# Kernel tuning notes

Hardware: AMD Instinct MI355X
Metric: run time of the kernel (lower is better)

## Reference

```python
import jax, jax.numpy as jnp
import numpy as np


def setup_inputs() -> dict:
    key = jax.random.key(0)
    ks = jax.random.split(key, 8)
    bs, slen, d = 16, 2048, 1024
    scale = 1.0 / np.sqrt(d)
    return {
        "query": jax.random.normal(ks[0], (bs, d), jnp.float32),
        "states": jax.random.normal(ks[1], (bs, slen, d), jnp.float32),
        "Wq": jax.random.normal(ks[2], (d, d), jnp.float32) * scale,
        "bq": jax.random.normal(ks[3], (d,), jnp.float32) * 0.01,
        "Wk": jax.random.normal(ks[4], (d, d), jnp.float32) * scale,
        "bk": jax.random.normal(ks[5], (d,), jnp.float32) * 0.01,
        "We": jax.random.normal(ks[6], (2 * d,), jnp.float32) * scale,
        "be": jax.random.normal(ks[7], (1,), jnp.float32) * 0.01,
    }


def reference(query, states, Wq, bq, Wk, bk, We, be):
    d = Wq.shape[1]
    # q: (bs, d); k: (bs, slen, d)
    q = jax.nn.relu(query @ Wq + bq)
    k = jax.nn.relu(jnp.einsum("bsv,vd->bsd", states, Wk) + bk)
    # tanh(cat(q, k)) @ We == tanh(q) @ We[:d] + tanh(k) @ We[d:]
    # (avoids materializing the repeated/concatenated (bs, slen, 2d) tensor)
    We_q, We_k = We[:d], We[d:]
    energy = (jnp.tanh(q) @ We_q)[:, None] + jnp.einsum("bsd,d->bs", jnp.tanh(k), We_k) + be[0]
    attn_weights = jax.nn.softmax(energy, axis=1)  # (bs, slen)
    attn = jnp.einsum("bs,bsd->bd", attn_weights, states)  # weighted sum of values
    return attn_weights, attn
```

## Files before the change

kernel.cpp:

```cpp
#include <hip/hip_runtime.h>
#include <hip/hip_bf16.h>

#define D 1024
#define SLEN 2048
#define BS 16
#define MROWS (BS*SLEN)

typedef __attribute__((ext_vector_type(8))) short short8;
typedef __attribute__((ext_vector_type(4))) float f32x4;

__device__ __forceinline__ short f2bf(float f) {
  __hip_bfloat16 h = __float2bfloat16(f);
  return __builtin_bit_cast(short, h);
}

__device__ __forceinline__ float4 ntload4(const float* p) {
  f32x4 v = __builtin_nontemporal_load((const f32x4*)p);
  float4 r; r.x = v.x; r.y = v.y; r.z = v.z; r.w = v.w; return r;
}

__global__ __launch_bounds__(256) void wk_prep(const float* __restrict__ Wk,
                                               short* __restrict__ WkT) {
  const int g = blockIdx.x;
  const int t = threadIdx.x;
#pragma unroll
  for (int it = 0; it < 4; ++it) {
    const int n = it*256 + t;
    short8 p;
#pragma unroll
    for (int j = 0; j < 8; ++j)
      p[j] = f2bf(Wk[(size_t)(g*8 + j)*D + n]);
    *(short8*)(WkT + ((size_t)g*D + n)*8) = p;
  }
}

__global__ __launch_bounds__(512, 2) void energy_gemm(
    const float* __restrict__ states, const short* __restrict__ WkT,
    const float* __restrict__ bk, const float* __restrict__ We,
    float* __restrict__ eraw, float* __restrict__ attn)
{
  __shared__ short Al[64 * 129 * 8];

  const int tid  = threadIdx.x;
  const int w    = tid >> 6;
  const int lane = tid & 63;
  const int quad = lane >> 4;
  const int l16  = lane & 15;
  const int m0   = blockIdx.x * 64;

  if (blockIdx.x < BS && tid < 256) {
    f32x4 z = {0.f, 0.f, 0.f, 0.f};
    *(f32x4*)(attn + (size_t)blockIdx.x*D + tid*4) = z;
  }

  {
    const int row = tid >> 3;
    const int u0  = tid & 7;
    const float* Ag = states + (size_t)(m0 + row)*D;
#pragma unroll
    for (int i = 0; i < 16; ++i) {
      const int u = u0 + i*8;
      float4 x0 = ntload4(Ag + u*8);
      float4 x1 = ntload4(Ag + u*8 + 4);
      short8 p;
      p[0]=f2bf(x0.x); p[1]=f2bf(x0.y); p[2]=f2bf(x0.z); p[3]=f2bf(x0.w);
      p[4]=f2bf(x1.x); p[5]=f2bf(x1.y); p[6]=f2bf(x1.z); p[7]=f2bf(x1.w);
      *(short8*)(Al + ((size_t)row*129 + u)*8) = p;
    }
  }
  __syncthreads();

  f32x4 acc[2][4][4];
#pragma unroll
  for (int nc = 0; nc < 2; ++nc)
#pragma unroll
    for (int mi = 0; mi < 4; ++mi)
#pragma unroll
      for (int ni = 0; ni < 4; ++ni)
        acc[nc][mi][ni] = (f32x4){0.f, 0.f, 0.f, 0.f};

  const short* bbase = WkT + ((size_t)quad*D + w*128 + l16)*8;
  const short* abase = Al + ((size_t)l16*129 + quad)*8;

#define LOADB(ks, buf)                                                   \
  {                                                                      \
    const short* bp = bbase + (size_t)(ks)*32768;                        \
    _Pragma("unroll")                                                    \
    for (int nc = 0; nc < 2; ++nc)                                       \
      _Pragma("unroll")                                                  \
      for (int ni = 0; ni < 4; ++ni)                                     \
        buf[nc*4 + ni] = *(const short8*)(bp + nc*512 + ni*128);         \
  }

#define LOADA(ks, buf)                                                   \
  {                                                                      \
    _Pragma("unroll")                                                    \
    for (int mi = 0; mi < 4; ++mi)                                       \
      buf[mi] = *(const short8*)(abase + mi*16512 + (ks)*32);            \
  }

#define MFMAS(fa, fb)                                                    \
  {                                                                      \
    _Pragma("unroll")                                                    \
    for (int nc = 0; nc < 2; ++nc)                                       \
      _Pragma("unroll")                                                  \
      for (int mi = 0; mi < 4; ++mi)                                     \
        _Pragma("unroll")                                                \
        for (int ni = 0; ni < 4; ++ni)                                   \
          acc[nc][mi][ni] = __builtin_amdgcn_mfma_f32_16x16x32_bf16(     \
              fa[mi], fb[nc*4 + ni], acc[nc][mi][ni], 0, 0, 0);          \
  }

  short8 fa0[4], fa1[4], fb0[8], fb1[8];
  LOADA(0, fa0); LOADB(0, fb0);
#pragma unroll
  for (int kk = 0; kk < 16; ++kk) {
    LOADA(2*kk + 1, fa1); LOADB(2*kk + 1, fb1);
    MFMAS(fa0, fb0);
    if (kk < 15) { LOADA(2*kk + 2, fa0); LOADB(2*kk + 2, fb0); }
    MFMAS(fa1, fb1);
  }

  float esum[16];
#pragma unroll
  for (int q = 0; q < 16; ++q) esum[q] = 0.f;
#pragma unroll
  for (int nc = 0; nc < 2; ++nc)
#pragma unroll
    for (int ni = 0; ni < 4; ++ni) {
      const int n = w*128 + nc*64 + ni*16 + l16;
      const float bkv = bk[n];
      const float wev = We[D + n];
#pragma unroll
      for (int mi = 0; mi < 4; ++mi)
#pragma unroll
        for (int r = 0; r < 4; ++r) {
          float x = acc[nc][mi][ni][r] + bkv;
          x = fmaxf(x, 0.f);
          float ex = __expf(2.f * x);
          float th = 1.f - 2.f/(ex + 1.f);
          esum[mi*4 + r] += th * wev;
        }
    }
#pragma unroll
  for (int dd = 1; dd < 16; dd <<= 1)
#pragma unroll
    for (int q = 0; q < 16; ++q)
      esum[q] += __shfl_xor(esum[q], dd, 64);

  __syncthreads();
  float* red = (float*)Al;
  if (l16 == 0) {
#pragma unroll
    for (int mi = 0; mi < 4; ++mi)
#pragma unroll
      for (int r = 0; r < 4; ++r)
        red[(mi*16 + quad*4 + r)*8 + w] = esum[mi*4 + r];
  }
  __syncthreads();
  if (tid < 64) {
    float s = 0.f;
#pragma unroll
    for (int wi = 0; wi < 8; ++wi) s += red[tid*8 + wi];
    eraw[m0 + tid] = s;
  }
#undef LOADB
#undef LOADA
#undef MFMAS
}

__global__ __launch_bounds__(256) void attn_sm_partial(
    const float* __restrict__ states, const float* __restrict__ eraw,
    float* __restrict__ wts, float* __restrict__ attn)
{
  const int sc = blockIdx.x;
  const int b  = blockIdx.y;
  const int t  = threadIdx.x;
  __shared__ float red[256];
  __shared__ float wsh[128];

  float v[8];
  float m = -1e30f;
#pragma unroll
  for (int j = 0; j < 8; ++j) {
    v[j] = eraw[(size_t)b*SLEN + j*256 + t];
    m = fmaxf(m, v[j]);
  }
  red[t] = m; __syncthreads();
  for (int s = 128; s > 0; s >>= 1) {
    if (t < s) red[t] = fmaxf(red[t], red[t+s]);
    __syncthreads();
  }
  m = red[0];
  __syncthreads();
  float sum = 0.f;
#pragma unroll
  for (int j = 0; j < 8; ++j) sum += __expf(v[j] - m);
  red[t] = sum; __syncthreads();
  for (int s = 128; s > 0; s >>= 1) {
    if (t < s) red[t] += red[t+s];
    __syncthreads();
  }
  const float inv = 1.f / red[0];

  if (t < 128) {
    const float wv = __expf(eraw[(size_t)b*SLEN + sc*128 + t] - m) * inv;
    wts[(size_t)b*SLEN + sc*128 + t] = wv;
    wsh[t] = wv;
  }
  __syncthreads();

  const float* sp = states + ((size_t)b*SLEN + sc*128)*D + t*4;
  float ax = 0.f, ay = 0.f, az = 0.f, aw = 0.f;
#pragma unroll 8
  for (int s = 0; s < 128; ++s) {
    float4 x = ntload4(sp + (size_t)s*D);
    const float wv = wsh[s];
    ax = fmaf(wv, x.x, ax);
    ay = fmaf(wv, x.y, ay);
    az = fmaf(wv, x.z, az);
    aw = fmaf(wv, x.w, aw);
  }
  float* o = attn + (size_t)b*D + t*4;
  atomicAdd(o+0, ax); atomicAdd(o+1, ay);
  atomicAdd(o+2, az); atomicAdd(o+3, aw);
}

extern "C" void kernel_launch(void* const* d_in, const int* in_sizes, int n_in,
                              void* d_out, int out_size, void* d_ws, size_t ws_size,
                              hipStream_t stream) {
  const float* states = (const float*)d_in[1];
  const float* Wk     = (const float*)d_in[4];
  const float* bk     = (const float*)d_in[5];
  const float* We     = (const float*)d_in[6];
  float* out = (float*)d_out;

  short* WkT  = (short*)d_ws;
  float* eraw = (float*)((char*)d_ws + (size_t)D*D*sizeof(short));

  (void)in_sizes; (void)n_in; (void)out_size; (void)ws_size;

  wk_prep<<<128, 256, 0, stream>>>(Wk, WkT);
  energy_gemm<<<MROWS/64, 512, 0, stream>>>(states, WkT, bk, We, eraw, out + MROWS);
  attn_sm_partial<<<dim3(16, BS), 256, 0, stream>>>(states, eraw, out, out + MROWS);
}
```

Baseline: 289.8 us.

## Split softmax from weighted sum and widen attention accumulation parallelism

Moves the per-batch softmax into its own small kernel so the weighted-sum kernel no longer recomputes the full softmax reduction in every block. The accumulation kernel now runs twice as many blocks, each with 512 threads covering two 32-row halves of a 64-row chunk, and combines the halves in shared memory before the atomics. States loads switch from nontemporal to normal loads, which may let them hit in cache after the GEMM pass. The cost is an extra kernel launch and a round trip of the weights through global memory.

New measurement: 301.7 us. 4.1% more time.

```diff
diff --git a/kernel.cpp b/kernel.cpp
--- a/kernel.cpp
+++ b/kernel.cpp
@@ -169,61 +169,81 @@
 #undef MFMAS
 }
 
-__global__ __launch_bounds__(256) void attn_sm_partial(
-    const float* __restrict__ states, const float* __restrict__ eraw,
-    float* __restrict__ wts, float* __restrict__ attn)
+__global__ __launch_bounds__(256) void softmax_w(
+    const float* __restrict__ eraw, float* __restrict__ wts)
+{
+  const int b = blockIdx.x;
+  const int t = threadIdx.x;
+  __shared__ float red[256];
+
+  float v[8];
+  float m = -1e30f;
+#pragma unroll
+  for (int j = 0; j < 8; ++j) {
+    v[j] = eraw[(size_t)b*SLEN + j*256 + t];
+    m = fmaxf(m, v[j]);
+  }
+  red[t] = m; __syncthreads();
+  for (int s = 128; s > 0; s >>= 1) {
+    if (t < s) red[t] = fmaxf(red[t], red[t+s]);
+    __syncthreads();
+  }
+  m = red[0];
+  __syncthreads();
+
+  float e[8];
+  float sum = 0.f;
+#pragma unroll
+  for (int j = 0; j < 8; ++j) { e[j] = __expf(v[j] - m); sum += e[j]; }
+  red[t] = sum; __syncthreads();
+  for (int s = 128; s > 0; s >>= 1) {
+    if (t < s) red[t] += red[t+s];
+    __syncthreads();
+  }
+  const float inv = 1.f / red[0];
+#pragma unroll
+  for (int j = 0; j < 8; ++j)
+    wts[(size_t)b*SLEN + j*256 + t] = e[j] * inv;
+}
+
+__global__ __launch_bounds__(512, 4) void attn_accum(
+    const float* __restrict__ states, const float* __restrict__ wts,
+    float* __restrict__ attn)
 {
   const int sc = blockIdx.x;
   const int b  = blockIdx.y;
   const int t  = threadIdx.x;
-  __shared__ float red[256];
-  __shared__ float wsh[128];
-
-  float v[8];
-  float m = -1e30f;
-#pragma unroll
-  for (int j = 0; j < 8; ++j) {
-    v[j] = eraw[(size_t)b*SLEN + j*256 + t];
-    m = fmaxf(m, v[j]);
-  }
-  red[t] = m; __syncthreads();
-  for (int s = 128; s > 0; s >>= 1) {
-    if (t < s) red[t] = fmaxf(red[t], red[t+s]);
-    __syncthreads();
-  }
-  m = red[0];
-  __syncthreads();
-  float sum = 0.f;
-#pragma unroll
-  for (int j = 0; j < 8; ++j) sum += __expf(v[j] - m);
-  red[t] = sum; __syncthreads();
-  for (int s = 128; s > 0; s >>= 1) {
-    if (t < s) red[t] += red[t+s];
-    __syncthreads();
-  }
-  const float inv = 1.f / red[0];
-
-  if (t < 128) {
-    const float wv = __expf(eraw[(size_t)b*SLEN + sc*128 + t] - m) * inv;
-    wts[(size_t)b*SLEN + sc*128 + t] = wv;
-    wsh[t] = wv;
-  }
-  __syncthreads();
-
-  const float* sp = states + ((size_t)b*SLEN + sc*128)*D + t*4;
+  const int dq = (t & 255) << 2;
+  const int ss = t >> 8;
+
+  __shared__ float  wsh[64];
+  __shared__ float4 part[256];
+
+  if (t < 64) wsh[t] = wts[(size_t)b*SLEN + sc*64 + t];
+  __syncthreads();
+
+  const float* sp = states + ((size_t)b*SLEN + sc*64 + ss*32)*D + dq;
   float ax = 0.f, ay = 0.f, az = 0.f, aw = 0.f;
-#pragma unroll 8
-  for (int s = 0; s < 128; ++s) {
-    float4 x = ntload4(sp + (size_t)s*D);
-    const float wv = wsh[s];
+#pragma unroll
+  for (int s = 0; s < 32; ++s) {
+    float4 x = *(const float4*)(sp + (size_t)s*D);
+    const float wv = wsh[ss*32 + s];
     ax = fmaf(wv, x.x, ax);
     ay = fmaf(wv, x.y, ay);
     az = fmaf(wv, x.z, az);
     aw = fmaf(wv, x.w, aw);
   }
-  float* o = attn + (size_t)b*D + t*4;
-  atomicAdd(o+0, ax); atomicAdd(o+1, ay);
-  atomicAdd(o+2, az); atomicAdd(o+3, aw);
+
+  if (ss) part[t & 255] = (float4){ax, ay, az, aw};
+  __syncthreads();
+  if (!ss) {
+    const float4 o = part[t];
+    float* p = attn + (size_t)b*D + dq;
+    atomicAdd(p + 0, ax + o.x);
+    atomicAdd(p + 1, ay + o.y);
+    atomicAdd(p + 2, az + o.z);
+    atomicAdd(p + 3, aw + o.w);
+  }
 }
 
 extern "C" void kernel_launch(void* const* d_in, const int* in_sizes, int n_in,
@@ -242,5 +262,6 @@
 
   wk_prep<<<128, 256, 0, stream>>>(Wk, WkT);
   energy_gemm<<<MROWS/64, 512, 0, stream>>>(states, WkT, bk, We, eraw, out + MROWS);
-  attn_sm_partial<<<dim3(16, BS), 256, 0, stream>>>(states, eraw, out, out + MROWS);
-}
+  softmax_w<<<BS, 256, 0, stream>>>(eraw, out);
+  attn_accum<<<dim3(32, BS), 512, 0, stream>>>(states, out, out + MROWS);
+}
```

## Fuse weighted-sum into energy GEMM using online-softmax partials per chunk

Applied to the files above, without the earlier changes.

The energy GEMM block now computes a per-chunk softmax max and sum, then forms a partial weighted sum of its 64 state rows directly from the bf16 tile already held in shared memory. A small finalize kernel rescales and combines the chunk partials and writes the normalized weights. This drops the second full fp32 read of states and the atomics. The trade-off is that the attention sum now uses bf16-rounded states, which lowers accuracy, and each GEMM block gains some extra epilogue work.

Result: faster. 274.2 us (-5.4%).

```diff
diff --git a/kernel.cpp b/kernel.cpp
--- a/kernel.cpp
+++ b/kernel.cpp
@@ -5,6 +5,7 @@
 #define SLEN 2048
 #define BS 16
 #define MROWS (BS*SLEN)
+#define NCHUNK (MROWS/64)
 
 typedef __attribute__((ext_vector_type(8))) short short8;
 typedef __attribute__((ext_vector_type(4))) float f32x4;
@@ -37,21 +38,20 @@
 __global__ __launch_bounds__(512, 2) void energy_gemm(
     const float* __restrict__ states, const short* __restrict__ WkT,
     const float* __restrict__ bk, const float* __restrict__ We,
-    float* __restrict__ eraw, float* __restrict__ attn)
+    float* __restrict__ eraw, float* __restrict__ pattn,
+    float* __restrict__ cmax, float* __restrict__ csum)
 {
   __shared__ short Al[64 * 129 * 8];
+  __shared__ float red2[64 * 8];
+  __shared__ float pfin[64];
 
   const int tid  = threadIdx.x;
   const int w    = tid >> 6;
   const int lane = tid & 63;
   const int quad = lane >> 4;
   const int l16  = lane & 15;
-  const int m0   = blockIdx.x * 64;
-
-  if (blockIdx.x < BS && tid < 256) {
-    f32x4 z = {0.f, 0.f, 0.f, 0.f};
-    *(f32x4*)(attn + (size_t)blockIdx.x*D + tid*4) = z;
-  }
+  const int g    = blockIdx.x;
+  const int m0   = g * 64;
 
   {
     const int row = tid >> 3;
@@ -148,82 +148,98 @@
     for (int q = 0; q < 16; ++q)
       esum[q] += __shfl_xor(esum[q], dd, 64);
 
-  __syncthreads();
-  float* red = (float*)Al;
   if (l16 == 0) {
 #pragma unroll
     for (int mi = 0; mi < 4; ++mi)
 #pragma unroll
       for (int r = 0; r < 4; ++r)
-        red[(mi*16 + quad*4 + r)*8 + w] = esum[mi*4 + r];
-  }
-  __syncthreads();
+        red2[(mi*16 + quad*4 + r)*8 + w] = esum[mi*4 + r];
+  }
+  __syncthreads();
+
   if (tid < 64) {
-    float s = 0.f;
-#pragma unroll
-    for (int wi = 0; wi < 8; ++wi) s += red[tid*8 + wi];
-    eraw[m0 + tid] = s;
+    float e = 0.f;
+#pragma unroll
+    for (int wi = 0; wi < 8; ++wi) e += red2[tid*8 + wi];
+    eraw[m0 + tid] = e;
+    float mm = e;
+#pragma unroll
+    for (int dd = 1; dd < 64; dd <<= 1) mm = fmaxf(mm, __shfl_xor(mm, dd, 64));
+    const float pv = __expf(e - mm);
+    float ss = pv;
+#pragma unroll
+    for (int dd = 1; dd < 64; dd <<= 1) ss += __shfl_xor(ss, dd, 64);
+    pfin[tid] = pv;
+    if (tid == 0) { cmax[g] = mm; csum[g] = ss; }
+  }
+  __syncthreads();
+
+  {
+    const int u    = tid >> 2;
+    const int joff = (tid & 3) * 2;
+    const short* ap = Al + (size_t)u*8 + joff;
+    float a0 = 0.f, a1 = 0.f;
+#pragma unroll 16
+    for (int row = 0; row < 64; ++row) {
+      const unsigned int bits = *(const unsigned int*)(ap + (size_t)row*1032);
+      const float pv = pfin[row];
+      const float lo = __builtin_bit_cast(float, bits << 16);
+      const float hi = __builtin_bit_cast(float, bits & 0xffff0000u);
+      a0 = fmaf(pv, lo, a0);
+      a1 = fmaf(pv, hi, a1);
+    }
+    float2 o; o.x = a0; o.y = a1;
+    *(float2*)(pattn + (size_t)g*D + 2*tid) = o;
   }
 #undef LOADB
 #undef LOADA
 #undef MFMAS
 }
 
-__global__ __launch_bounds__(256) void attn_sm_partial(
-    const float* __restrict__ states, const float* __restrict__ eraw,
+__global__ __launch_bounds__(256) void attn_finalize(
+    const float* __restrict__ eraw, const float* __restrict__ pattn,
+    const float* __restrict__ cmax, const float* __restrict__ csum,
     float* __restrict__ wts, float* __restrict__ attn)
 {
-  const int sc = blockIdx.x;
-  const int b  = blockIdx.y;
-  const int t  = threadIdx.x;
-  __shared__ float red[256];
-  __shared__ float wsh[128];
-
-  float v[8];
-  float m = -1e30f;
+  const int b = blockIdx.x;
+  const int t = threadIdx.x;
+  __shared__ float scl[32];
+  __shared__ float stats[2];
+
+  if (t < 32) {
+    const float m = cmax[b*32 + t];
+    float mm = m;
+#pragma unroll
+    for (int dd = 1; dd < 32; dd <<= 1) mm = fmaxf(mm, __shfl_xor(mm, dd, 64));
+    const float e = __expf(m - mm);
+    scl[t] = e;
+    float s = e * csum[b*32 + t];
+#pragma unroll
+    for (int dd = 1; dd < 32; dd <<= 1) s += __shfl_xor(s, dd, 64);
+    if (t == 0) { stats[0] = mm; stats[1] = 1.f / s; }
+  }
+  __syncthreads();
+  const float m_b = stats[0];
+  const float inv = stats[1];
+
 #pragma unroll
   for (int j = 0; j < 8; ++j) {
-    v[j] = eraw[(size_t)b*SLEN + j*256 + t];
-    m = fmaxf(m, v[j]);
-  }
-  red[t] = m; __syncthreads();
-  for (int s = 128; s > 0; s >>= 1) {
-    if (t < s) red[t] = fmaxf(red[t], red[t+s]);
-    __syncthreads();
-  }
-  m = red[0];
-  __syncthreads();
-  float sum = 0.f;
-#pragma unroll
-  for (int j = 0; j < 8; ++j) sum += __expf(v[j] - m);
-  red[t] = sum; __syncthreads();
-  for (int s = 128; s > 0; s >>= 1) {
-    if (t < s) red[t] += red[t+s];
-    __syncthreads();
-  }
-  const float inv = 1.f / red[0];
-
-  if (t < 128) {
-    const float wv = __expf(eraw[(size_t)b*SLEN + sc*128 + t] - m) * inv;
-    wts[(size_t)b*SLEN + sc*128 + t] = wv;
-    wsh[t] = wv;
-  }
-  __syncthreads();
-
-  const float* sp = states + ((size_t)b*SLEN + sc*128)*D + t*4;
-  float ax = 0.f, ay = 0.f, az = 0.f, aw = 0.f;
-#pragma unroll 8
-  for (int s = 0; s < 128; ++s) {
-    float4 x = ntload4(sp + (size_t)s*D);
-    const float wv = wsh[s];
-    ax = fmaf(wv, x.x, ax);
-    ay = fmaf(wv, x.y, ay);
-    az = fmaf(wv, x.z, az);
-    aw = fmaf(wv, x.w, aw);
-  }
-  float* o = attn + (size_t)b*D + t*4;
-  atomicAdd(o+0, ax); atomicAdd(o+1, ay);
-  atomicAdd(o+2, az); atomicAdd(o+3, aw);
+    const int s = j*256 + t;
+    wts[(size_t)b*SLEN + s] = __expf(eraw[(size_t)b*SLEN + s] - m_b) * inv;
+  }
+
+  float acc[4] = {0.f, 0.f, 0.f, 0.f};
+#pragma unroll
+  for (int c = 0; c < 32; ++c) {
+    const float sc = scl[c];
+    const float* pp = pattn + ((size_t)(b*32 + c))*D + t;
+#pragma unroll
+    for (int j = 0; j < 4; ++j)
+      acc[j] = fmaf(sc, pp[j*256], acc[j]);
+  }
+#pragma unroll
+  for (int j = 0; j < 4; ++j)
+    attn[(size_t)b*D + j*256 + t] = acc[j] * inv;
 }
 
 extern "C" void kernel_launch(void* const* d_in, const int* in_sizes, int n_in,
@@ -235,12 +251,16 @@
   const float* We     = (const float*)d_in[6];
   float* out = (float*)d_out;
 
-  short* WkT  = (short*)d_ws;
-  float* eraw = (float*)((char*)d_ws + (size_t)D*D*sizeof(short));
+  char* ws = (char*)d_ws;
+  short* WkT   = (short*)ws;                                  ws += (size_t)D*D*sizeof(short);
+  float* eraw  = (float*)ws;                                  ws += (size_t)MROWS*sizeof(float);
+  float* pattn = (float*)ws;                                  ws += (size_t)NCHUNK*D*sizeof(float);
+  float* cmaxp = (float*)ws;                                  ws += (size_t)NCHUNK*sizeof(float);
+  float* csump = (float*)ws;
 
   (void)in_sizes; (void)n_in; (void)out_size; (void)ws_size;
 
   wk_prep<<<128, 256, 0, stream>>>(Wk, WkT);
-  energy_gemm<<<MROWS/64, 512, 0, stream>>>(states, WkT, bk, We, eraw, out + MROWS);
-  attn_sm_partial<<<dim3(16, BS), 256, 0, stream>>>(states, eraw, out, out + MROWS);
-}
+  energy_gemm<<<NCHUNK, 512, 0, stream>>>(states, WkT, bk, We, eraw, pattn, cmaxp, csump);
+  attn_finalize<<<BS, 256, 0, stream>>>(eraw, pattn, cmaxp, csump, out, out + MROWS);
+}
```
